# Optimization experiments

Hardware: AMD Instinct MI355X
Metric: run time of the kernel (lower is better)

Reference implementation:

```python
import jax, jax.numpy as jnp
import numpy as np

D = 384      # d_model
NH = 8       # num_heads
HW = 96      # spatial h = w
RATIOS = (4, 8, 16)


def _p2i(x):
    # (hg wg b) c h w -> b c (hg h) (wg w), hg=wg=2, b=1
    f, c, h, w = x.shape
    return x.reshape(2, 2, c, h, w).transpose(2, 0, 3, 1, 4).reshape(1, c, 2 * h, 2 * w)


def _i2p(x):
    # b c (hg h) (wg w) -> (hg wg b) c h w, hg=wg=2, b=1
    _, c, H2, W2 = x.shape
    h, w = H2 // 2, W2 // 2
    return x.reshape(c, 2, h, 2, w).transpose(1, 3, 0, 2, 4).reshape(4, c, h, w)


def _ln(x, g, b, eps=1e-5):
    m = x.mean(-1, keepdims=True)
    v = ((x - m) ** 2).mean(-1, keepdims=True)
    return (x - m) * jax.lax.rsqrt(v + eps) * g + b


def setup_inputs() -> dict:
    key = jax.random.key(0)
    ks = jax.random.split(key, 8)
    rn = lambda k, s: jax.random.normal(k, s, dtype=jnp.float32) * 0.02
    return {
        "x": jax.random.normal(ks[0], (5, D, HW, HW), dtype=jnp.float32),
        "sal_w": rn(ks[1], (1, D)),
        "sal_b": jnp.zeros((1,), jnp.float32),
        "attn_in_w": rn(ks[2], (4, 3 * D, D)),
        "attn_in_b": jnp.zeros((4, 3 * D), jnp.float32),
        "attn_out_w": rn(ks[3], (4, D, D)),
        "attn_out_b": jnp.zeros((4, D), jnp.float32),
        "w3": rn(ks[4], (2 * D, D)),
        "b3": jnp.zeros((2 * D,), jnp.float32),
        "w4": rn(ks[5], (D, 2 * D)),
        "b4": jnp.zeros((D,), jnp.float32),
        "g1": jnp.ones((D,), jnp.float32),
        "be1": jnp.zeros((D,), jnp.float32),
        "g2": jnp.ones((D,), jnp.float32),
        "be2": jnp.zeros((D,), jnp.float32),
    }


def reference(x, sal_w, sal_b, attn_in_w, attn_in_b, attn_out_w, attn_out_b,
              w3, b3, w4, b4, g1, be1, g2, be2):
    b, c, h, w = x.shape
    loc, glb = x[:4], x[4:5]                      # (4,c,h,w), (1,c,h,w)
    pg = _i2p(glb)                                # (4,c,h/2,w/2)

    tam = jax.nn.sigmoid(jnp.einsum('oc,chw->ohw', sal_w, glb[0]) + sal_b[:, None, None])  # (1,h,w)
    tam_up = jnp.repeat(jnp.repeat(tam, 2, axis=1), 2, axis=2)[None]                        # (1,1,2h,2w)
    loc = loc * _i2p(tam_up)                      # (4,c,h,w) * (4,1,h,w)

    # multi-ratio adaptive average pooling of patched global (sizes divide exactly)
    pools = []
    for r in RATIOS:
        th, tw = round(h / r), round(w / r)
        kh, kw = (h // 2) // th, (w // 2) // tw
        p = pg.reshape(4, c, th, kh, tw, kw).mean((3, 5))
        pools.append(p.reshape(4, c, th * tw))
    kv = jnp.concatenate(pools, axis=2).transpose(0, 2, 1)   # (4,S,c)

    q = loc.reshape(4, c, h * w).transpose(0, 2, 1)          # (4,L,c)

    # 4 independent MHA blocks, vectorized over the patch dim n
    dh = c // NH
    wq, wk, wv = attn_in_w[:, :c], attn_in_w[:, c:2 * c], attn_in_w[:, 2 * c:]
    bq, bk, bv = attn_in_b[:, :c], attn_in_b[:, c:2 * c], attn_in_b[:, 2 * c:]
    heads = lambda t: t.reshape(4, -1, NH, dh).transpose(0, 2, 1, 3)
    qh = heads(jnp.einsum('nlc,ndc->nld', q, wq) + bq[:, None, :])
    kh = heads(jnp.einsum('nsc,ndc->nsd', kv, wk) + bk[:, None, :])
    vh = heads(jnp.einsum('nsc,ndc->nsd', kv, wv) + bv[:, None, :])
    scores = jnp.einsum('nhld,nhsd->nhls', qh, kh) / jnp.sqrt(jnp.float32(dh))
    attn = jax.nn.softmax(scores, axis=-1)
    ao = jnp.einsum('nhls,nhsd->nhld', attn, vh).transpose(0, 2, 1, 3).reshape(4, -1, c)
    ao = jnp.einsum('nlc,ndc->nld', ao, attn_out_w) + attn_out_b[:, None, :]  # (4,L,c)
    outputs = ao.transpose(1, 0, 2)                                           # (L,4,c)

    # residual + FFN block (dropouts are identity in eval)
    src = loc.reshape(4, c, -1).transpose(2, 0, 1) + outputs                  # (L,4,c)
    src = _ln(src, g1, be1)
    hid = jax.nn.gelu(jnp.einsum('lnc,dc->lnd', src, w3) + b3, approximate=False)
    ff = jnp.einsum('lnd,cd->lnc', hid, w4) + b4
    src = _ln(src + ff, g2, be2)
    src = src.transpose(1, 2, 0).reshape(4, c, h, w)

    # nearest-downsample (factor 2) of stitched patches, add to global
    glb = glb + _p2i(src)[:, :, ::2, ::2]
    return jnp.concatenate([src, glb], axis=0)
```

## Files before the change

### kernel.cpp

```cpp
#include <hip/hip_runtime.h>

typedef __attribute__((ext_vector_type(8))) __bf16 bf16x8;
typedef __attribute__((ext_vector_type(4))) __bf16 bf16x4;
typedef __attribute__((ext_vector_type(4))) float f32x4;

__device__ __forceinline__ bf16x8 zero8() {
  bf16x8 z;
#pragma unroll
  for (int i = 0; i < 8; ++i) z[i] = (__bf16)0.f;
  return z;
}

__device__ __forceinline__ float wave_sum(float v) {
#pragma unroll
  for (int off = 1; off < 64; off <<= 1) v += __shfl_xor(v, off);
  return v;
}

__device__ __forceinline__ void gll(const __bf16* g, __bf16* l) {
  __builtin_amdgcn_global_load_lds(
      (const __attribute__((address_space(1))) void*)g,
      (__attribute__((address_space(3))) void*)l, 16, 0, 0);
}

__global__ __launch_bounds__(256) void k_cvt4(const float* __restrict__ a,
    const float* __restrict__ b, const float* __restrict__ c, const float* __restrict__ d,
    __bf16* __restrict__ oa, __bf16* __restrict__ ob, __bf16* __restrict__ oc,
    __bf16* __restrict__ od) {
  const int i = blockIdx.x * 256 + threadIdx.x;
  const float* src; __bf16* dst; int off;
  if (i < 442368)      { src = a; dst = oa; off = i; }
  else if (i < 589824) { src = b; dst = ob; off = i - 442368; }
  else if (i < 663552) { src = c; dst = oc; off = i - 589824; }
  else if (i < 737280) { src = d; dst = od; off = i - 663552; }
  else return;
  const f32x4 v = ((const f32x4*)src)[off];
  bf16x4 o;
#pragma unroll
  for (int e = 0; e < 4; ++e) o[e] = (__bf16)v[e];
  ((bf16x4*)dst)[off] = o;
}

__global__ __launch_bounds__(256) void k_tam(const float* __restrict__ x,
    const float* __restrict__ sal_w, const float* __restrict__ sal_b,
    float* __restrict__ tam) {
  const int lane = threadIdx.x & 63, w = threadIdx.x >> 6;
  const int pix = blockIdx.x * 64 + lane;
  const float* g = x + (size_t)4 * 384 * 9216;
  float acc = 0.f;
  for (int c = w * 96; c < w * 96 + 96; ++c)
    acc += sal_w[c] * g[(size_t)c * 9216 + pix];
  __shared__ float part[4][64];
  part[w][lane] = acc;
  __syncthreads();
  if (w == 0) {
    float v = part[0][lane] + part[1][lane] + part[2][lane] + part[3][lane] + sal_b[0];
    tam[pix] = 1.f / (1.f + __expf(-v));
  }
}

__global__ __launch_bounds__(256) void k_locscale(const float* __restrict__ x,
    const float* __restrict__ tam, __bf16* __restrict__ Q) {
  const int n = blockIdx.y;
  const int l0 = blockIdx.x * 64;
  const int tid = threadIdx.x;
  __shared__ float tile[64][69];
  const size_t bx = (size_t)n * 384 * 9216;
  const int a = n >> 1, b = n & 1;
  for (int c0 = 0; c0 < 384; c0 += 64) {
    if (c0) __syncthreads();
#pragma unroll
    for (int pass = 0; pass < 4; ++pass) {
      int cc = pass * 16 + (tid >> 4);
      int ll = (tid & 15) * 4;
      f32x4 v = *(const f32x4*)&x[bx + (size_t)(c0 + cc) * 9216 + l0 + ll];
#pragma unroll
      for (int e = 0; e < 4; ++e) tile[cc][ll + e] = v[e];
    }
    __syncthreads();
    const int ll = tid >> 2, c1 = (tid & 3) * 16;
    const int l = l0 + ll, i = l / 96, j = l % 96;
    const float tv = tam[(a * 48 + (i >> 1)) * 96 + b * 48 + (j >> 1)];
    const size_t orow = ((size_t)n * 9216 + l) * 384 + c0 + c1;
#pragma unroll
    for (int cc = 0; cc < 16; ++cc)
      Q[orow + cc] = (__bf16)(tile[c1 + cc][ll] * tv);
  }
}

__global__ __launch_bounds__(64) void k_pool(const float* __restrict__ x,
    __bf16* __restrict__ KV) {
  const int c = blockIdx.x, n = blockIdx.y;
  const int a = n >> 1, b = n & 1;
  const float* g = x + (size_t)(4 * 384 + c) * 9216;
  __shared__ float quad[48][48];
  const int t = threadIdx.x;
  for (int k = t; k < 2304; k += 64) {
    int i = k / 48, j = k % 48;
    quad[i][j] = g[(a * 48 + i) * 96 + b * 48 + j];
  }
  __syncthreads();
  for (int s = t; s < 768; s += 64) {
    float val = 0.f;
    if (s < 576) {
      int ti = s / 24, tj = s % 24;
#pragma unroll
      for (int di = 0; di < 2; ++di)
#pragma unroll
        for (int dj = 0; dj < 2; ++dj) val += quad[ti * 2 + di][tj * 2 + dj];
      val *= 0.25f;
    } else if (s < 720) {
      int q = s - 576; int ti = q / 12, tj = q % 12;
      for (int di = 0; di < 4; ++di)
        for (int dj = 0; dj < 4; ++dj) val += quad[ti * 4 + di][tj * 4 + dj];
      val *= (1.f / 16.f);
    } else if (s < 756) {
      int q = s - 720; int ti = q / 6, tj = q % 6;
      for (int di = 0; di < 8; ++di)
        for (int dj = 0; dj < 8; ++dj) val += quad[ti * 8 + di][tj * 8 + dj];
      val *= (1.f / 64.f);
    }
    KV[((size_t)n * 768 + s) * 384 + c] = (__bf16)val;
  }
}

template <int GELU>
__global__ __launch_bounds__(256) void k_gemm(const __bf16* __restrict__ A,
    const __bf16* __restrict__ B, const float* __restrict__ bias,
    __bf16* __restrict__ C, int K, long sA, long sB, long sBias, long sC,
    float scale) {
  const int z = blockIdx.z;
  A += (size_t)z * sA; B += (size_t)z * sB; bias += (size_t)z * sBias; C += (size_t)z * sC;
  const int m0 = blockIdx.y * 128, n0 = blockIdx.x * 128;
  const int N = gridDim.x * 128;
  __shared__ __bf16 As[128 * 64], Bs[128 * 64];
  const int tid = threadIdx.x, lane = tid & 63, w = tid >> 6;
  const int wm = w >> 1, wn = w & 1;
  const int li = lane & 15, gq = lane >> 4;
  const int lrow = lane >> 3, lcol = (lane & 7) * 8;
  f32x4 acc[4][4] = {};
  const int nk = K >> 6;
  for (int kt = 0; kt < nk; ++kt) {
    const int k0 = kt * 64;
#pragma unroll
    for (int i = 0; i < 4; ++i) {
      const int r0 = w * 32 + i * 8;
      gll(A + (size_t)(m0 + r0 + lrow) * K + k0 + lcol, &As[r0 * 64]);
      gll(B + (size_t)(n0 + r0 + lrow) * K + k0 + lcol, &Bs[r0 * 64]);
    }
    __syncthreads();
#pragma unroll
    for (int kk = 0; kk < 2; ++kk) {
      bf16x8 af[4], bfr[4];
#pragma unroll
      for (int f = 0; f < 4; ++f) {
        af[f] = *(const bf16x8*)&As[(wm * 64 + f * 16 + li) * 64 + kk * 32 + gq * 8];
        bfr[f] = *(const bf16x8*)&Bs[(wn * 64 + f * 16 + li) * 64 + kk * 32 + gq * 8];
      }
#pragma unroll
      for (int fm = 0; fm < 4; ++fm)
#pragma unroll
        for (int fn = 0; fn < 4; ++fn)
          acc[fm][fn] = __builtin_amdgcn_mfma_f32_16x16x32_bf16(af[fm], bfr[fn], acc[fm][fn], 0, 0, 0);
    }
    __syncthreads();
  }
  float bv[4];
#pragma unroll
  for (int fn = 0; fn < 4; ++fn) bv[fn] = bias[n0 + wn * 64 + fn * 16 + li];
#pragma unroll
  for (int fm = 0; fm < 4; ++fm) {
    const int row = m0 + wm * 64 + fm * 16 + gq * 4;
#pragma unroll
    for (int fn = 0; fn < 4; ++fn) {
      const int col = n0 + wn * 64 + fn * 16 + li;
#pragma unroll
      for (int r = 0; r < 4; ++r) {
        float v = (acc[fm][fn][r] + bv[fn]) * scale;
        if (GELU) v = 0.5f * v * (1.f + erff(v * 0.70710678118654752f));
        C[(size_t)(row + r) * N + col] = (__bf16)v;
      }
    }
  }
}

__global__ __launch_bounds__(256) void k_kmax(const __bf16* __restrict__ KVH,
    float* __restrict__ kmax) {
  const int nh = blockIdx.x, n = nh >> 3, h = nh & 7;
  const size_t bk = (size_t)n * 768 * 768 + h * 48;
  const int tid = threadIdx.x;
  float m = 0.f;
  for (int s = tid; s < 756; s += 256) {
    float a2 = 0.f;
#pragma unroll
    for (int ch = 0; ch < 6; ++ch) {
      bf16x8 kv = *(const bf16x8*)&KVH[bk + (size_t)s * 768 + ch * 8];
#pragma unroll
      for (int e = 0; e < 8; ++e) { const float f = (float)kv[e]; a2 += f * f; }
    }
    m = fmaxf(m, a2);
  }
#pragma unroll
  for (int off = 1; off < 64; off <<= 1) m = fmaxf(m, __shfl_xor(m, off));
  __shared__ float red[4];
  if ((tid & 63) == 0) red[tid >> 6] = m;
  __syncthreads();
  if (tid == 0) kmax[nh] = fmaxf(fmaxf(red[0], red[1]), fmaxf(red[2], red[3]));
}

__global__ __launch_bounds__(256) void k_vt(const __bf16* __restrict__ KVH,
    __bf16* __restrict__ VT) {
  const int nh = blockIdx.y, n = nh >> 3, h = nh & 7;
  const int s0 = blockIdx.x * 256;
  __shared__ __bf16 tile[48][264];
  const int tid = threadIdx.x;
  const size_t bv = (size_t)n * 768 * 768 + 384 + h * 48;
#pragma unroll
  for (int it = 0; it < 6; ++it) {
    const int task = tid + it * 256;
    const int s = task / 6, ch = task % 6;
    bf16x8 v = *(const bf16x8*)&KVH[bv + (size_t)(s0 + s) * 768 + ch * 8];
#pragma unroll
    for (int e = 0; e < 8; ++e) tile[ch * 8 + e][s] = v[e];
  }
  __syncthreads();
#pragma unroll
  for (int it = 0; it < 6; ++it) {
    const int task = tid + it * 256;
    const int d = task >> 5, so = (task & 31) * 8;
    bf16x8 v2 = *(const bf16x8*)&tile[d][so];
    *(bf16x8*)&VT[((size_t)nh * 48 + d) * 768 + s0 + so] = v2;
  }
}

__global__ __launch_bounds__(512) void k_attn(const __bf16* __restrict__ QH,
    const __bf16* __restrict__ KVH, const __bf16* __restrict__ VT,
    const float* __restrict__ kmax, __bf16* __restrict__ AO) {
  const int nh = blockIdx.y, n = nh >> 3, h = nh & 7;
  const int l0 = blockIdx.x * 128;
  const int tid = threadIdx.x, lane = tid & 63, w = tid >> 6;
  const int gq = lane >> 4, li = lane & 15;
  const int l0w = l0 + w * 16;
  __shared__ __bf16 Ks[64 * 64];
  __shared__ __bf16 Vs[48 * 64];
  __shared__ __bf16 P[8][16 * 68];
  __bf16* Pw = &P[w][0];
  const size_t bq = ((size_t)n * 9216) * 384 + h * 48;
  const size_t bk = (size_t)n * 768 * 768 + h * 48;
  const __bf16* vt = VT + (size_t)nh * 48 * 768;
  const int scol = 8 * ((lane & 7) ^ (lane >> 3));
  const int rsw = 8 * (li & 7);
  bf16x8 qf[2];
#pragma unroll
  for (int kk = 0; kk < 2; ++kk) {
    const int d0 = kk * 32 + gq * 8;
    qf[kk] = (d0 < 48) ? *(const bf16x8*)&QH[bq + (size_t)(l0w + li) * 384 + d0] : zero8();
  }
  float q2 = 0.f;
#pragma unroll
  for (int kk = 0; kk < 2; ++kk)
#pragma unroll
    for (int e = 0; e < 8; ++e) { const float f = (float)qf[kk][e]; q2 += f * f; }
  q2 += __shfl_xor(q2, 16);
  q2 += __shfl_xor(q2, 32);
  const float m_fix = sqrtf(q2 * kmax[nh]);
  float l_run = 0.f;
  f32x4 o[3] = {};
  for (int t = 0; t < 12; ++t) {
    const int s0 = t * 64;
    __syncthreads();
    {
      const int rbase = w * 8;
      gll(KVH + bk + (size_t)(s0 + rbase + (lane >> 3)) * 768 + scol, &Ks[rbase * 64]);
    }
    if (w < 6) {
      const int rbase = w * 8;
      gll(vt + (size_t)(rbase + (lane >> 3)) * 768 + s0 + scol, &Vs[rbase * 64]);
    }
    __syncthreads();
    f32x4 sc[4];
#pragma unroll
    for (int st = 0; st < 4; ++st) {
      f32x4 a = {};
#pragma unroll
      for (int kk = 0; kk < 2; ++kk) {
        const bf16x8 kf = *(const bf16x8*)&Ks[(st * 16 + li) * 64 + ((kk * 32 + gq * 8) ^ rsw)];
        a = __builtin_amdgcn_mfma_f32_16x16x32_bf16(kf, qf[kk], a, 0, 0, 0);
      }
      sc[st] = a;
    }
    if (t == 11) {
#pragma unroll
      for (int st = 0; st < 4; ++st)
#pragma unroll
        for (int r = 0; r < 4; ++r)
          if (st * 16 + gq * 4 + r >= 52) sc[st][r] = -1e30f;
    }
#pragma unroll
    for (int st = 0; st < 4; ++st)
#pragma unroll
      for (int r = 0; r < 4; ++r) {
        const float p = __builtin_amdgcn_exp2f(sc[st][r] - m_fix);
        sc[st][r] = p;
        l_run += p;
      }
#pragma unroll
    for (int st = 0; st < 4; ++st) {
      bf16x4 pk;
#pragma unroll
      for (int r = 0; r < 4; ++r) pk[r] = (__bf16)sc[st][r];
      *(bf16x4*)&Pw[li * 68 + st * 16 + gq * 4] = pk;
    }
#pragma unroll
    for (int kk = 0; kk < 2; ++kk) {
      const bf16x4 plo = *(const bf16x4*)&Pw[li * 68 + kk * 32 + gq * 8];
      const bf16x4 phi = *(const bf16x4*)&Pw[li * 68 + kk * 32 + gq * 8 + 4];
      bf16x8 ap;
#pragma unroll
      for (int e = 0; e < 4; ++e) { ap[e] = plo[e]; ap[e + 4] = phi[e]; }
#pragma unroll
      for (int df = 0; df < 3; ++df) {
        const bf16x8 bv = *(const bf16x8*)&Vs[(df * 16 + li) * 64 + ((kk * 32 + gq * 8) ^ rsw)];
        o[df] = __builtin_amdgcn_mfma_f32_16x16x32_bf16(ap, bv, o[df], 0, 0, 0);
      }
    }
  }
  l_run += __shfl_xor(l_run, 16);
  l_run += __shfl_xor(l_run, 32);
  const float inv = 1.f / l_run;
  float ir[4];
#pragma unroll
  for (int r = 0; r < 4; ++r) ir[r] = __shfl(inv, gq * 4 + r, 16);
#pragma unroll
  for (int df = 0; df < 3; ++df)
#pragma unroll
    for (int r = 0; r < 4; ++r)
      AO[bq + (size_t)(l0w + gq * 4 + r) * 384 + df * 16 + li] = (__bf16)(o[df][r] * ir[r]);
}

__global__ __launch_bounds__(256) void k_ln1(const __bf16* Q,
    const __bf16* P, const float* g1, const float* b1, __bf16* S1) {
  const size_t row = (size_t)blockIdx.x * 4 + (threadIdx.x >> 6);
  const int lane = threadIdx.x & 63;
  const __bf16* q = Q + row * 384;
  const __bf16* p = P + row * 384;
  float v[6], s = 0.f;
#pragma unroll
  for (int e = 0; e < 6; ++e) {
    const int c = e * 64 + lane;
    v[e] = (float)q[c] + (float)p[c];
    s += v[e];
  }
  s = wave_sum(s);
  const float mean = s * (1.f / 384.f);
  float var = 0.f;
#pragma unroll
  for (int e = 0; e < 6; ++e) { const float d = v[e] - mean; var += d * d; }
  var = wave_sum(var) * (1.f / 384.f);
  const float rstd = rsqrtf(var + 1e-5f);
  __bf16* o = S1 + row * 384;
#pragma unroll
  for (int e = 0; e < 6; ++e) {
    const int c = e * 64 + lane;
    o[c] = (__bf16)(((v[e] - mean) * rstd) * g1[c] + b1[c]);
  }
}

__global__ __launch_bounds__(256) void k_ln2(const __bf16* __restrict__ S1,
    const __bf16* __restrict__ FF, const float* __restrict__ g2,
    const float* __restrict__ b2, float* __restrict__ out) {
  const int n = blockIdx.y, l0 = blockIdx.x * 64;
  const int tid = threadIdx.x, w = tid >> 6, lane = tid & 63;
  __shared__ __bf16 tile[64][390];
  for (int rr = 0; rr < 16; ++rr) {
    const int ll = w * 16 + rr;
    const size_t row = ((size_t)n * 9216 + l0 + ll) * 384;
    float v[6], s = 0.f;
#pragma unroll
    for (int e = 0; e < 6; ++e) {
      const int c = e * 64 + lane;
      v[e] = (float)S1[row + c] + (float)FF[row + c];
      s += v[e];
    }
    s = wave_sum(s);
    const float mean = s * (1.f / 384.f);
    float var = 0.f;
#pragma unroll
    for (int e = 0; e < 6; ++e) { const float d = v[e] - mean; var += d * d; }
    var = wave_sum(var) * (1.f / 384.f);
    const float rstd = rsqrtf(var + 1e-5f);
#pragma unroll
    for (int e = 0; e < 6; ++e) {
      const int c = e * 64 + lane;
      tile[ll][c] = (__bf16)(((v[e] - mean) * rstd) * g2[c] + b2[c]);
    }
  }
  __syncthreads();
  for (int it = 0; it < 96; ++it) {
    const int c = it * 4 + w;
    out[((size_t)n * 384 + c) * 9216 + l0 + lane] = (float)tile[lane][c];
  }
}

__global__ __launch_bounds__(256) void k_glb(const float* __restrict__ x,
    float* out) {
  const int gl = blockIdx.x * 64 + (threadIdx.x & 63);
  const int c = blockIdx.y * 4 + (threadIdx.x >> 6);
  const int y = gl / 96, xx = gl % 96;
  const int np = ((y / 48) << 1) + (xx / 48);
  const int ls = ((y % 48) * 2) * 96 + (xx % 48) * 2;
  const float v = x[(size_t)(4 * 384 + c) * 9216 + gl] +
                  out[((size_t)np * 384 + c) * 9216 + ls];
  out[(size_t)(4 * 384 + c) * 9216 + gl] = v;
}

extern "C" void kernel_launch(void* const* d_in, const int* in_sizes, int n_in,
                              void* d_out, int out_size, void* d_ws, size_t ws_size,
                              hipStream_t stream) {
  const float* x     = (const float*)d_in[0];
  const float* sal_w = (const float*)d_in[1];
  const float* sal_b = (const float*)d_in[2];
  const float* aiw   = (const float*)d_in[3];
  const float* aib   = (const float*)d_in[4];
  const float* aow   = (const float*)d_in[5];
  const float* aob   = (const float*)d_in[6];
  const float* w3    = (const float*)d_in[7];
  const float* b3    = (const float*)d_in[8];
  const float* w4    = (const float*)d_in[9];
  const float* b4    = (const float*)d_in[10];
  const float* g1    = (const float*)d_in[11];
  const float* be1   = (const float*)d_in[12];
  const float* g2    = (const float*)d_in[13];
  const float* be2   = (const float*)d_in[14];
  float* out = (float*)d_out;
  char* ws = (char*)d_ws;

  float*  tam  = (float*)(ws + 0);
  __bf16* aiwB = (__bf16*)(ws + 36864);
  __bf16* aowB = (__bf16*)(ws + 3575808);
  __bf16* w3B  = (__bf16*)(ws + 4755456);
  __bf16* w4B  = (__bf16*)(ws + 5345280);
  __bf16* KV   = (__bf16*)(ws + 5935104);
  __bf16* KVH  = (__bf16*)(ws + 8294400);
  __bf16* Q    = (__bf16*)(ws + 13012992);
  __bf16* QHb  = (__bf16*)(ws + 41324544);
  __bf16* VTg = KV;
  __bf16* AO  = (__bf16*)d_out;
  __bf16* HID = (__bf16*)d_out;
  float* kmax = (float*)((char*)d_out + 70778368);
  __bf16* P   = QHb;
  __bf16* S1  = Q;
  __bf16* FF  = QHb;

  const float qscale = 0.20823509f;

  k_cvt4<<<2880, 256, 0, stream>>>(aiw, aow, w3, w4, aiwB, aowB, w3B, w4B);

  k_tam<<<144, 256, 0, stream>>>(x, sal_w, sal_b, tam);
  k_locscale<<<dim3(144, 4), 256, 0, stream>>>(x, tam, Q);
  k_pool<<<dim3(384, 4), 64, 0, stream>>>(x, KV);

  k_gemm<0><<<dim3(6, 6, 4), 256, 0, stream>>>(KV, aiwB + 384 * 384, aib + 384, KVH,
      384, 768L * 384, 1152L * 384, 1152L, 768L * 768, 1.f);
  k_gemm<0><<<dim3(3, 72, 4), 256, 0, stream>>>(Q, aiwB, aib, QHb,
      384, 9216L * 384, 1152L * 384, 1152L, 9216L * 384, qscale);

  k_kmax<<<32, 256, 0, stream>>>(KVH, kmax);
  k_vt<<<dim3(3, 32), 256, 0, stream>>>(KVH, VTg);

  k_attn<<<dim3(72, 32), 512, 0, stream>>>(QHb, KVH, VTg, kmax, AO);

  k_gemm<0><<<dim3(3, 72, 4), 256, 0, stream>>>(AO, aowB, aob, P,
      384, 9216L * 384, 384L * 384, 384L, 9216L * 384, 1.f);

  k_ln1<<<9216, 256, 0, stream>>>(Q, P, g1, be1, S1);

  k_gemm<1><<<dim3(6, 288, 1), 256, 0, stream>>>(S1, w3B, b3, HID,
      384, 0, 0, 0, 0, 1.f);
  k_gemm<0><<<dim3(3, 288, 1), 256, 0, stream>>>(HID, w4B, b4, FF,
      768, 0, 0, 0, 0, 1.f);

  k_ln2<<<dim3(144, 4), 256, 0, stream>>>(S1, FF, g2, be2, out);
  k_glb<<<dim3(144, 96), 256, 0, stream>>>(x, out);
}
```

Baseline: 346.1 us.

## Double-buffer K/V tiles in attention and fold row-sum into PV MFMA

The attention kernel now double-buffers the K and V shared-memory tiles, prefetching the next 64-key tile with global_load_lds while computing on the current one, which halves the barriers per iteration. It also removes the scalar softmax denominator accumulation and instead appends a constant row of ones to the V tile, so a fourth PV MFMA produces the row sums of the bf16-rounded probabilities. This costs more shared memory and one extra MFMA per k-step, and the denominator now sums bf16-rounded values rather than fp32 ones.

```diff
diff --git a/kernel.cpp b/kernel.cpp
--- a/kernel.cpp
+++ b/kernel.cpp
@@ -241,8 +241,8 @@
   const int tid = threadIdx.x, lane = tid & 63, w = tid >> 6;
   const int gq = lane >> 4, li = lane & 15;
   const int l0w = l0 + w * 16;
-  __shared__ __bf16 Ks[64 * 64];
-  __shared__ __bf16 Vs[48 * 64];
+  __shared__ __bf16 Ks[2][64 * 64];
+  __shared__ __bf16 Vs[2][64 * 64];
   __shared__ __bf16 P[8][16 * 68];
   __bf16* Pw = &P[w][0];
   const size_t bq = ((size_t)n * 9216) * 384 + h * 48;
@@ -250,6 +250,14 @@
   const __bf16* vt = VT + (size_t)nh * 48 * 768;
   const int scol = 8 * ((lane & 7) ^ (lane >> 3));
   const int rsw = 8 * (li & 7);
+  {
+    const int idx = tid & 255, buf = tid >> 8;
+    const int row = 48 + (idx >> 4), col = (idx & 15) * 4;
+    bf16x4 cv;
+#pragma unroll
+    for (int e = 0; e < 4; ++e) cv[e] = (__bf16)(row == 48 ? 1.f : 0.f);
+    *(bf16x4*)&Vs[buf][row * 64 + col] = cv;
+  }
   bf16x8 qf[2];
 #pragma unroll
   for (int kk = 0; kk < 2; ++kk) {
@@ -264,27 +272,26 @@
   q2 += __shfl_xor(q2, 16);
   q2 += __shfl_xor(q2, 32);
   const float m_fix = sqrtf(q2 * kmax[nh]);
-  float l_run = 0.f;
-  f32x4 o[3] = {};
+  f32x4 o[4] = {};
+  gll(KVH + bk + (size_t)(w * 8 + (lane >> 3)) * 768 + scol, &Ks[0][w * 8 * 64]);
+  if (w < 6)
+    gll(vt + (size_t)(w * 8 + (lane >> 3)) * 768 + 0 + scol, &Vs[0][w * 8 * 64]);
+  __syncthreads();
   for (int t = 0; t < 12; ++t) {
-    const int s0 = t * 64;
-    __syncthreads();
-    {
-      const int rbase = w * 8;
-      gll(KVH + bk + (size_t)(s0 + rbase + (lane >> 3)) * 768 + scol, &Ks[rbase * 64]);
-    }
-    if (w < 6) {
-      const int rbase = w * 8;
-      gll(vt + (size_t)(rbase + (lane >> 3)) * 768 + s0 + scol, &Vs[rbase * 64]);
-    }
-    __syncthreads();
+    const int cur = t & 1, nxt = cur ^ 1;
+    if (t < 11) {
+      const int s1 = (t + 1) * 64;
+      gll(KVH + bk + (size_t)(s1 + w * 8 + (lane >> 3)) * 768 + scol, &Ks[nxt][w * 8 * 64]);
+      if (w < 6)
+        gll(vt + (size_t)(w * 8 + (lane >> 3)) * 768 + s1 + scol, &Vs[nxt][w * 8 * 64]);
+    }
     f32x4 sc[4];
 #pragma unroll
     for (int st = 0; st < 4; ++st) {
       f32x4 a = {};
 #pragma unroll
       for (int kk = 0; kk < 2; ++kk) {
-        const bf16x8 kf = *(const bf16x8*)&Ks[(st * 16 + li) * 64 + ((kk * 32 + gq * 8) ^ rsw)];
+        const bf16x8 kf = *(const bf16x8*)&Ks[cur][(st * 16 + li) * 64 + ((kk * 32 + gq * 8) ^ rsw)];
         a = __builtin_amdgcn_mfma_f32_16x16x32_bf16(kf, qf[kk], a, 0, 0, 0);
       }
       sc[st] = a;
@@ -297,18 +304,10 @@
           if (st * 16 + gq * 4 + r >= 52) sc[st][r] = -1e30f;
     }
 #pragma unroll
-    for (int st = 0; st < 4; ++st)
-#pragma unroll
-      for (int r = 0; r < 4; ++r) {
-        const float p = __builtin_amdgcn_exp2f(sc[st][r] - m_fix);
-        sc[st][r] = p;
-        l_run += p;
-      }
-#pragma unroll
     for (int st = 0; st < 4; ++st) {
       bf16x4 pk;
 #pragma unroll
-      for (int r = 0; r < 4; ++r) pk[r] = (__bf16)sc[st][r];
+      for (int r = 0; r < 4; ++r) pk[r] = (__bf16)__builtin_amdgcn_exp2f(sc[st][r] - m_fix);
       *(bf16x4*)&Pw[li * 68 + st * 16 + gq * 4] = pk;
     }
 #pragma unroll
@@ -319,18 +318,16 @@
 #pragma unroll
       for (int e = 0; e < 4; ++e) { ap[e] = plo[e]; ap[e + 4] = phi[e]; }
 #pragma unroll
-      for (int df = 0; df < 3; ++df) {
-        const bf16x8 bv = *(const bf16x8*)&Vs[(df * 16 + li) * 64 + ((kk * 32 + gq * 8) ^ rsw)];
+      for (int df = 0; df < 4; ++df) {
+        const bf16x8 bv = *(const bf16x8*)&Vs[cur][(df * 16 + li) * 64 + ((kk * 32 + gq * 8) ^ rsw)];
         o[df] = __builtin_amdgcn_mfma_f32_16x16x32_bf16(ap, bv, o[df], 0, 0, 0);
       }
     }
-  }
-  l_run += __shfl_xor(l_run, 16);
-  l_run += __shfl_xor(l_run, 32);
-  const float inv = 1.f / l_run;
+    __syncthreads();
+  }
   float ir[4];
 #pragma unroll
-  for (int r = 0; r < 4; ++r) ir[r] = __shfl(inv, gq * 4 + r, 16);
+  for (int r = 0; r < 4; ++r) ir[r] = 1.f / __shfl(o[3][r], lane & 48);
 #pragma unroll
   for (int df = 0; df < 3; ++df)
 #pragma unroll
```

After: 348.3 us. Within noise of the previous version (+0.6%).
